# Optimization experiments

Hardware: AMD Instinct MI355X
Metric: run time of the kernel (lower is better)

Reference implementation:

```python
import jax, jax.numpy as jnp
import numpy as np

HS = WS = 1024      # downsampled mask dims (8192 / scale_factor 8)
K = 24              # kernel_num
KD = 35             # kernel_dim1 == kernel_dim2
OFF = HS // 2 - KD // 2  # offset_s = 495
MASK_STEEP = 4.0
MASK_SHIFT = 0.5
RESIST_STEEP = 50.0
RESIST_TH = 0.225
MAX_DOSE = 1.02
MIN_DOSE = 0.98
POOL = 3            # avepool_kernel


def setup_inputs() -> dict:
    key = jax.random.key(0)
    ks = jax.random.split(key, 7)
    return {
        "mask_s": jax.random.uniform(ks[0], (1, 1, HS, WS), dtype=jnp.float32),
        "kf_re": jax.random.normal(ks[1], (K, KD, KD), dtype=jnp.float32),
        "kf_im": jax.random.normal(ks[2], (K, KD, KD), dtype=jnp.float32),
        "kd_re": jax.random.normal(ks[3], (K, KD, KD), dtype=jnp.float32),
        "kd_im": jax.random.normal(ks[4], (K, KD, KD), dtype=jnp.float32),
        "kf_scale": jax.random.uniform(ks[5], (K, 1, 1), dtype=jnp.float32),
        "kd_scale": jax.random.uniform(ks[6], (K, 1, 1), dtype=jnp.float32),
    }


def _avgpool3(x):
    # AvgPool2d(kernel=3, stride=1, pad=1), count_include_pad=True -> always /9
    s = jax.lax.reduce_window(x, 0.0, jax.lax.add, (1, 1, POOL, POOL),
                              (1, 1, 1, 1),
                              [(0, 0), (0, 0), (POOL // 2, POOL // 2), (POOL // 2, POOL // 2)])
    return s / float(POOL * POOL)


def _dose_branch(crop, kernel, scale, dose):
    # crop: [1,1,KD,KD] complex ; kernel: [K,KD,KD] complex ; scale: [K,1,1]
    buf = jnp.zeros((1, K, HS, WS), dtype=jnp.complex64)
    buf = buf.at[:, :, OFF:OFF + KD, OFF:OFF + KD].set(crop * dose * kernel)
    img = jnp.fft.ifft2(buf)                      # [1,K,HS,WS] complex
    inten = (img.real * img.real + img.imag * img.imag) * scale
    inten = jnp.sum(inten, axis=1, keepdims=True)  # [1,1,HS,WS]
    return jax.nn.sigmoid(RESIST_STEEP * (inten - RESIST_TH))


def reference(mask_s, kf_re, kf_im, kd_re, kd_im, kf_scale, kd_scale):
    kf = jax.lax.complex(kf_re, kf_im)
    kd = jax.lax.complex(kd_re, kd_im)
    mask = jax.nn.sigmoid(MASK_STEEP * (_avgpool3(mask_s) - MASK_SHIFT))
    mf = jnp.fft.fftshift(jnp.fft.fft2(mask), axes=(-2, -1))  # [1,1,HS,WS]
    crop = mf[:, :, OFF:OFF + KD, OFF:OFF + KD]               # [1,1,KD,KD]
    x_nom = _dose_branch(crop, kf, kf_scale, 1.0)
    x_max = _dose_branch(crop, kf, kf_scale, MAX_DOSE)
    x_min = _dose_branch(crop, kd, kd_scale, MIN_DOSE)
    return x_nom, x_max, x_min
```

## Files before the change

kernel.cpp:

```cpp
#include <hip/hip_runtime.h>
#include <math.h>

#define HS 1024
#define WS 1024
#define KK 24
#define KD 35
#define NF 35
#define NDP 69
#define NGRP 16
#define CROW 42
#define NCHUNK 38
#define PRS 10

#define G_OFF    0u
#define CROP_OFF 286720u
#define D_OFF    296520u
#define ZERO_QWORDS 6055

__global__ __launch_bounds__(256) void k_maskG(const float* __restrict__ ms,
                                               float2* __restrict__ G,
                                               unsigned long long* __restrict__ zq) {
    __shared__ float cs[WS + 8];
    __shared__ float m[WS];
    __shared__ float2 part[252];
    const int x = blockIdx.x;
    const int t = threadIdx.x;

    if (x < 24) {
        int i = x * 256 + t;
        if (i < ZERO_QWORDS) zq[i] = 0ull;
    }
    {
        const int j = 4 * t;
        float4 b = *(const float4*)&ms[x * WS + j];
        float4 a = make_float4(0.f, 0.f, 0.f, 0.f);
        float4 d = make_float4(0.f, 0.f, 0.f, 0.f);
        if (x > 0)      a = *(const float4*)&ms[(x - 1) * WS + j];
        if (x < HS - 1) d = *(const float4*)&ms[(x + 1) * WS + j];
        float4 s;
        s.x = a.x + b.x + d.x;
        s.y = a.y + b.y + d.y;
        s.z = a.z + b.z + d.z;
        s.w = a.w + b.w + d.w;
        *(float4*)&cs[4 + j] = s;
        if (t == 0) { cs[3] = 0.0f; cs[4 + WS] = 0.0f; }
    }
    __syncthreads();
    {
        const int j = 4 * t;
        float4 c = *(const float4*)&cs[4 + j];
        float l = cs[3 + j];
        float r = cs[8 + j];
        float p0 = (l   + c.x + c.y) * (1.0f / 9.0f);
        float p1 = (c.x + c.y + c.z) * (1.0f / 9.0f);
        float p2 = (c.y + c.z + c.w) * (1.0f / 9.0f);
        float p3 = (c.z + c.w + r  ) * (1.0f / 9.0f);
        float4 mv;
        mv.x = 1.0f / (1.0f + expf(-4.0f * (p0 - 0.5f)));
        mv.y = 1.0f / (1.0f + expf(-4.0f * (p1 - 0.5f)));
        mv.z = 1.0f / (1.0f + expf(-4.0f * (p2 - 0.5f)));
        mv.w = 1.0f / (1.0f + expf(-4.0f * (p3 - 0.5f)));
        *(float4*)&m[j] = mv;
    }
    __syncthreads();
    if (t < 252) {
        const int qi = t / 14, seg = t % 14;
        float si, ci, ss, cc;
        sincospif(-(float)(qi * seg) * (1.0f / 512.0f), &si, &ci);
        sincospif(-(float)(qi * 14)  * (1.0f / 512.0f), &ss, &cc);
        const float s2 = (qi & 1) ? -1.0f : 1.0f;
        const int qm = qi & 3;
        const float er = (qm == 0) ? 1.0f : (qm == 2) ? -1.0f : 0.0f;
        const float ei = (qm == 1) ? -1.0f : (qm == 3) ? 1.0f : 0.0f;
        float wr = ci, wi = si;
        float re = 0.0f, im = 0.0f;
        for (int y = seg; y < 256; y += 14) {
            float m0 = m[y], m1 = m[y + 256], m2 = m[y + 512], m3 = m[y + 768];
            float A  = fmaf(s2, m2, m0);
            float Bv = fmaf(s2, m3, m1);
            float tre = fmaf(er, Bv, A);
            float tim = ei * Bv;
            re += tre * wr - tim * wi;
            im += tre * wi + tim * wr;
            float nr = wr * cc - wi * ss;
            wi = wr * ss + wi * cc;
            wr = nr;
        }
        part[t] = make_float2(re, im);
    }
    __syncthreads();
    if (t < 18) {
        float re = 0.0f, im = 0.0f;
        for (int s = 0; s < 14; ++s) { float2 p = part[t * 14 + s]; re += p.x; im += p.y; }
        G[(17 + t) * HS + x] = make_float2(re, im);
        if (t > 0) G[(17 - t) * HS + x] = make_float2(re, -im);
    }
}

__global__ __launch_bounds__(256) void k_crop(const float2* __restrict__ G,
                                              float2* __restrict__ crop) {
    __shared__ float2 g2[64];
    __shared__ float2 part[245];
    const int q  = blockIdx.x >> 4;
    const int xs = (blockIdx.x & 15) * 64;
    const int t  = threadIdx.x;
    if (t < 64) g2[t] = G[q * HS + xs + t];
    __syncthreads();
    if (t < 245) {
        const int p = t / 7, seg = t % 7;
        const int v = p - 17;
        float si, ci, ss, cc;
        sincospif((float)(v * (xs + seg)) * (1.0f / 512.0f), &si, &ci);
        sincospif((float)(v * 7)          * (1.0f / 512.0f), &ss, &cc);
        float wr = ci, wi = si;
        float re = 0.0f, im = 0.0f;
        for (int r = seg; r < 64; r += 7) {
            float2 gv = g2[r];
            re += gv.x * wr + gv.y * wi;
            im += gv.y * wr - gv.x * wi;
            float nr = wr * cc - wi * ss;
            wi = wr * ss + wi * cc;
            wr = nr;
        }
        part[t] = make_float2(re, im);
    }
    __syncthreads();
    if (t < NF) {
        float re = 0.0f, im = 0.0f;
        for (int s = 0; s < 7; ++s) { float2 p2 = part[t * 7 + s]; re += p2.x; im += p2.y; }
        float* dst = (float*)&crop[t * NF + q];
        atomicAdd(dst,     re);
        atomicAdd(dst + 1, im);
    }
}

__global__ __launch_bounds__(256) void k_D(
    const float2* __restrict__ crop,
    const float* __restrict__ kre0, const float* __restrict__ kim0,
    const float* __restrict__ kre1, const float* __restrict__ kim1,
    const float* __restrict__ sc0,  const float* __restrict__ sc1,
    float2* __restrict__ D)
{
    __shared__ float2 C[KD * CROW];
    __shared__ float partRf[2][NCHUNK * 6 * PRS];
    const int tup = blockIdx.x;
    const int t   = threadIdx.x;

    const int b   = tup / (KK * NGRP);
    const int rem = tup % (KK * NGRP);
    const int k   = rem / NGRP;
    const int g   = rem % NGRP;
    const float* kre = b ? kre1 : kre0;
    const float* kim = b ? kim1 : kim0;
    const float dosefac = (b ? 0.98f : 1.0f) * (1.0f / 1048576.0f);
    const float sk2 = ((b ? sc1 : sc0)[k]) * dosefac * dosefac;

    if (t < 245) C[(t / 7) * CROW + 35 + (t % 7)] = make_float2(0.0f, 0.0f);
    #pragma unroll
    for (int j = 0; j < 5; ++j) {
        int i = t + j * 256;
        if (i < KD * KD) {
            float2 c = crop[i];
            int row = i / 35, col = i % 35;
            float kr = kre[k * KD * KD + i], ki = kim[k * KD * KD + i];
            C[row * CROW + col] = make_float2(c.x * kr - c.y * ki,
                                              c.x * ki + c.y * kr);
        }
    }
    __syncthreads();

    const int ch = t / 6;
    const int pg = t % 6;
    const bool act = (ch < NCHUNK);
    const int tau = (ch >= 7) + (ch >= 14) + (ch >= 20) + (ch >= 25)
                  + (ch >= 29) + (ch >= 32) + (ch >= 35) + (ch >= 37);
    const int cbt = (tau == 0) ? 0 : (tau == 1) ? 7 : (tau == 2) ? 14 : (tau == 3) ? 20
                  : (tau == 4) ? 25 : (tau == 5) ? 29 : (tau == 6) ? 32 : (tau == 7) ? 35 : 37;
    const int d0 = 4 * tau;
    const int u0 = 5 * (ch - cbt);

    const int tau2 = t >> 2;
    const int cb2 = (tau2 == 0) ? 0 : (tau2 == 1) ? 7 : (tau2 == 2) ? 14 : (tau2 == 3) ? 20
                  : (tau2 == 4) ? 25 : (tau2 == 5) ? 29 : (tau2 == 6) ? 32 : (tau2 == 7) ? 35 : 37;
    const int cn2 = (tau2 == 0) ? 7 : (tau2 == 1) ? 7 : (tau2 == 2) ? 6 : (tau2 == 3) ? 5
                  : (tau2 == 4) ? 4 : (tau2 == 5) ? 3 : (tau2 == 6) ? 3 : (tau2 == 7) ? 2 : 1;
    const int s0 = cb2 * 6, cnt = cn2 * 6, c2 = (t & 3) * 2;

    int pb = 0;
    for (int idp = g; idp < NDP; idp += NGRP) {
        const int dp = idp - 34;
        if (act) {
            const int plo = max(0, dp), phi = min(34, 34 + dp);
            float2 ac0 = {0,0}, ac1 = {0,0}, ac2 = {0,0}, ac3 = {0,0};
            for (int p = plo + pg; p <= phi; p += 6) {
                const float2* rowa = &C[p * CROW + d0 + u0];
                const float2* rowb = &C[(p - dp) * CROW + u0];
                float2 a0 = rowa[0], a1 = rowa[1], a2 = rowa[2];
                #pragma unroll
                for (int s = 0; s < 5; ++s) {
                    float2 a3 = rowa[s + 3];
                    float2 bb = rowb[s];
                    ac0.x += a0.x * bb.x + a0.y * bb.y;  ac0.y += a0.y * bb.x - a0.x * bb.y;
                    ac1.x += a1.x * bb.x + a1.y * bb.y;  ac1.y += a1.y * bb.x - a1.x * bb.y;
                    ac2.x += a2.x * bb.x + a2.y * bb.y;  ac2.y += a2.y * bb.x - a2.x * bb.y;
                    ac3.x += a3.x * bb.x + a3.y * bb.y;  ac3.y += a3.y * bb.x - a3.x * bb.y;
                    a0 = a1; a1 = a2; a2 = a3;
                }
            }
            float* pr = &partRf[pb][t * PRS];
            *(float2*)&pr[0] = ac0;
            *(float2*)&pr[2] = ac1;
            *(float2*)&pr[4] = ac2;
            *(float2*)&pr[6] = ac3;
        }
        __syncthreads();
        if (t < NF) {
            float re = 0.0f, im = 0.0f;
            for (int j = 0; j < cnt; ++j) {
                const float2 v = *(const float2*)&partRf[pb][(s0 + j) * PRS + c2];
                re += v.x; im += v.y;
            }
            float* dst = (float*)&D[(b * NDP + idp) * NF + t];
            atomicAdd(dst,     re * sk2);
            atomicAdd(dst + 1, im * sk2);
        }
        pb ^= 1;
    }
}

__global__ __launch_bounds__(256) void k_final(const float2* __restrict__ D,
                                               float* __restrict__ out) {
    __shared__ float2 partB[210];
    __shared__ float2 B[NF][2];
    const int x = blockIdx.x;
    const int t = threadIdx.x;
    if (t < 210) {
        const int s = t / 70, r = t % 70, b = r / 35, dq = r % 35;
        float si, ci, ss, cc;
        sincospif((float)((23 * s - 34) * x) * (1.0f / 512.0f), &si, &ci);
        sincospif((float)x                   * (1.0f / 512.0f), &ss, &cc);
        float wr = ci, wi = si;
        float re = 0.0f, im = 0.0f;
        const int i0 = 23 * s;
        for (int idp = i0; idp < i0 + 23; ++idp) {
            float2 d = D[(b * NDP + idp) * NF + dq];
            re += d.x * wr - d.y * wi;
            im += d.x * wi + d.y * wr;
            float nr = wr * cc - wi * ss;
            wi = wr * ss + wi * cc;
            wr = nr;
        }
        partB[t] = make_float2(re, im);
    }
    __syncthreads();
    if (t < 70) {
        float2 a = partB[t], b2 = partB[t + 70], c = partB[t + 140];
        B[t % 35][t / 35] = make_float2(a.x + b2.x + c.x, a.y + b2.y + c.y);
    }
    __syncthreads();
    const float bf0 = B[0][0].x;
    const float bd0 = B[0][1].x;
    float s1, c1;
    sincospif((float)t * (1.0f / 512.0f), &s1, &c1);
    float cx = c1, cy = s1;
    float2 Sf[4] = {{0,0},{0,0},{0,0},{0,0}};
    float2 Sd[4] = {{0,0},{0,0},{0,0},{0,0}};
    #pragma unroll
    for (int dq = 1; dq < NF; ++dq) {
        const float2 bf = B[dq][0];
        const float2 bd = B[dq][1];
        const int mm = dq & 3;
        Sf[mm].x += bf.x * cx - bf.y * cy;
        Sf[mm].y += bf.x * cy + bf.y * cx;
        Sd[mm].x += bd.x * cx - bd.y * cy;
        Sd[mm].y += bd.x * cy + bd.y * cx;
        const float nx = cx * c1 - cy * s1;
        cy = cx * s1 + cy * c1;
        cx = nx;
    }
    float sf[4], sd[4];
    sf[0] = Sf[0].x + Sf[1].x + Sf[2].x + Sf[3].x;
    sf[1] = Sf[0].x - Sf[1].y - Sf[2].x + Sf[3].y;
    sf[2] = Sf[0].x - Sf[1].x + Sf[2].x - Sf[3].x;
    sf[3] = Sf[0].x + Sf[1].y - Sf[2].x - Sf[3].y;
    sd[0] = Sd[0].x + Sd[1].x + Sd[2].x + Sd[3].x;
    sd[1] = Sd[0].x - Sd[1].y - Sd[2].x + Sd[3].y;
    sd[2] = Sd[0].x - Sd[1].x + Sd[2].x - Sd[3].x;
    sd[3] = Sd[0].x + Sd[1].y - Sd[2].x - Sd[3].y;
    #pragma unroll
    for (int j = 0; j < 4; ++j) {
        const float If = bf0 + 2.0f * sf[j];
        const float Id = bd0 + 2.0f * sd[j];
        const int o = x * WS + t + 256 * j;
        out[o]               = 1.0f / (1.0f + expf(-50.0f * (If - 0.225f)));
        out[o + HS * WS]     = 1.0f / (1.0f + expf(-50.0f * (1.0404f * If - 0.225f)));
        out[o + 2 * HS * WS] = 1.0f / (1.0f + expf(-50.0f * (Id - 0.225f)));
    }
}

extern "C" void kernel_launch(void* const* d_in, const int* in_sizes, int n_in,
                              void* d_out, int out_size, void* d_ws, size_t ws_size,
                              hipStream_t stream) {
    (void)in_sizes; (void)n_in; (void)out_size; (void)ws_size;
    const float* ms    = (const float*)d_in[0];
    const float* kf_re = (const float*)d_in[1];
    const float* kf_im = (const float*)d_in[2];
    const float* kd_re = (const float*)d_in[3];
    const float* kd_im = (const float*)d_in[4];
    const float* kf_sc = (const float*)d_in[5];
    const float* kd_sc = (const float*)d_in[6];

    char* ws = (char*)d_ws;
    float2* G      = (float2*)(ws + G_OFF);
    float2* crop   = (float2*)(ws + CROP_OFF);
    float2* D      = (float2*)(ws + D_OFF);
    unsigned long long* zq = (unsigned long long*)(ws + CROP_OFF);
    float* out     = (float*)d_out;

    k_maskG<<<HS, 256, 0, stream>>>(ms, G, zq);
    k_crop<<<NF * 16, 256, 0, stream>>>(G, crop);
    k_D<<<2 * KK * NGRP, 256, 0, stream>>>(crop, kf_re, kf_im, kd_re, kd_im, kf_sc, kd_sc, D);
    k_final<<<HS, 256, 0, stream>>>(D, out);
}
```

Baseline: 48.94 us.

## Use Chebyshev twiddle recurrence, split crop blocks finer, spread D reduction across waves

```diff
diff --git a/kernel.cpp b/kernel.cpp
--- a/kernel.cpp
+++ b/kernel.cpp
@@ -72,7 +72,10 @@
         const int qm = qi & 3;
         const float er = (qm == 0) ? 1.0f : (qm == 2) ? -1.0f : 0.0f;
         const float ei = (qm == 1) ? -1.0f : (qm == 3) ? 1.0f : 0.0f;
+        const float tc = 2.0f * cc;
         float wr = ci, wi = si;
+        float pr = ci * cc + si * ss;
+        float pi = si * cc - ci * ss;
         float re = 0.0f, im = 0.0f;
         for (int y = seg; y < 256; y += 14) {
             float m0 = m[y], m1 = m[y + 256], m2 = m[y + 512], m3 = m[y + 768];
@@ -82,9 +85,9 @@
             float tim = ei * Bv;
             re += tre * wr - tim * wi;
             im += tre * wi + tim * wr;
-            float nr = wr * cc - wi * ss;
-            wi = wr * ss + wi * cc;
-            wr = nr;
+            float nr = tc * wr - pr;
+            float ni = tc * wi - pi;
+            pr = wr; pi = wi; wr = nr; wi = ni;
         }
         part[t] = make_float2(re, im);
     }
@@ -99,12 +102,12 @@
 
 __global__ __launch_bounds__(256) void k_crop(const float2* __restrict__ G,
                                               float2* __restrict__ crop) {
-    __shared__ float2 g2[64];
+    __shared__ float2 g2[32];
     __shared__ float2 part[245];
-    const int q  = blockIdx.x >> 4;
-    const int xs = (blockIdx.x & 15) * 64;
+    const int q  = blockIdx.x >> 5;
+    const int xs = (blockIdx.x & 31) * 32;
     const int t  = threadIdx.x;
-    if (t < 64) g2[t] = G[q * HS + xs + t];
+    if (t < 32) g2[t] = G[q * HS + xs + t];
     __syncthreads();
     if (t < 245) {
         const int p = t / 7, seg = t % 7;
@@ -112,15 +115,18 @@
         float si, ci, ss, cc;
         sincospif((float)(v * (xs + seg)) * (1.0f / 512.0f), &si, &ci);
         sincospif((float)(v * 7)          * (1.0f / 512.0f), &ss, &cc);
+        const float tc = 2.0f * cc;
         float wr = ci, wi = si;
-        float re = 0.0f, im = 0.0f;
-        for (int r = seg; r < 64; r += 7) {
+        float pr = ci * cc + si * ss;
+        float pi = si * cc - ci * ss;
+        float re = 0.0f, im = 0.0f;
+        for (int r = seg; r < 32; r += 7) {
             float2 gv = g2[r];
             re += gv.x * wr + gv.y * wi;
             im += gv.y * wr - gv.x * wi;
-            float nr = wr * cc - wi * ss;
-            wi = wr * ss + wi * cc;
-            wr = nr;
+            float nr = tc * wr - pr;
+            float ni = tc * wi - pi;
+            pr = wr; pi = wi; wr = nr; wi = ni;
         }
         part[t] = make_float2(re, im);
     }
@@ -179,12 +185,15 @@
     const int d0 = 4 * tau;
     const int u0 = 5 * (ch - cbt);
 
-    const int tau2 = t >> 2;
-    const int cb2 = (tau2 == 0) ? 0 : (tau2 == 1) ? 7 : (tau2 == 2) ? 14 : (tau2 == 3) ? 20
-                  : (tau2 == 4) ? 25 : (tau2 == 5) ? 29 : (tau2 == 6) ? 32 : (tau2 == 7) ? 35 : 37;
-    const int cn2 = (tau2 == 0) ? 7 : (tau2 == 1) ? 7 : (tau2 == 2) ? 6 : (tau2 == 3) ? 5
-                  : (tau2 == 4) ? 4 : (tau2 == 5) ? 3 : (tau2 == 6) ? 3 : (tau2 == 7) ? 2 : 1;
-    const int s0 = cb2 * 6, cnt = cn2 * 6, c2 = (t & 3) * 2;
+    const int w4 = t >> 6;
+    const int ix = t & 63;
+    const int dqr = 4 * ix + w4;
+    const bool ract = (ix < 9) && (dqr < NF);
+    const int cb2 = (ix == 0) ? 0 : (ix == 1) ? 7 : (ix == 2) ? 14 : (ix == 3) ? 20
+                  : (ix == 4) ? 25 : (ix == 5) ? 29 : (ix == 6) ? 32 : (ix == 7) ? 35 : 37;
+    const int cn2 = (ix == 0) ? 7 : (ix == 1) ? 7 : (ix == 2) ? 6 : (ix == 3) ? 5
+                  : (ix == 4) ? 4 : (ix == 5) ? 3 : (ix == 6) ? 3 : (ix == 7) ? 2 : 1;
+    const int s0 = cb2 * 6, cnt = cn2 * 6, c2 = w4 * 2;
 
     int pb = 0;
     for (int idp = g; idp < NDP; idp += NGRP) {
@@ -214,13 +223,13 @@
             *(float2*)&pr[6] = ac3;
         }
         __syncthreads();
-        if (t < NF) {
+        if (ract) {
             float re = 0.0f, im = 0.0f;
             for (int j = 0; j < cnt; ++j) {
                 const float2 v = *(const float2*)&partRf[pb][(s0 + j) * PRS + c2];
                 re += v.x; im += v.y;
             }
-            float* dst = (float*)&D[(b * NDP + idp) * NF + t];
+            float* dst = (float*)&D[(b * NDP + idp) * NF + dqr];
             atomicAdd(dst,     re * sk2);
             atomicAdd(dst + 1, im * sk2);
         }
@@ -239,16 +248,19 @@
         float si, ci, ss, cc;
         sincospif((float)((23 * s - 34) * x) * (1.0f / 512.0f), &si, &ci);
         sincospif((float)x                   * (1.0f / 512.0f), &ss, &cc);
+        const float tc = 2.0f * cc;
         float wr = ci, wi = si;
+        float pr = ci * cc + si * ss;
+        float pi = si * cc - ci * ss;
         float re = 0.0f, im = 0.0f;
         const int i0 = 23 * s;
         for (int idp = i0; idp < i0 + 23; ++idp) {
             float2 d = D[(b * NDP + idp) * NF + dq];
             re += d.x * wr - d.y * wi;
             im += d.x * wi + d.y * wr;
-            float nr = wr * cc - wi * ss;
-            wi = wr * ss + wi * cc;
-            wr = nr;
+            float nr = tc * wr - pr;
+            float ni = tc * wi - pi;
+            pr = wr; pi = wi; wr = nr; wi = ni;
         }
         partB[t] = make_float2(re, im);
     }
@@ -262,7 +274,9 @@
     const float bd0 = B[0][1].x;
     float s1, c1;
     sincospif((float)t * (1.0f / 512.0f), &s1, &c1);
+    const float tc = 2.0f * c1;
     float cx = c1, cy = s1;
+    float px = 1.0f, py = 0.0f;
     float2 Sf[4] = {{0,0},{0,0},{0,0},{0,0}};
     float2 Sd[4] = {{0,0},{0,0},{0,0},{0,0}};
     #pragma unroll
@@ -274,9 +288,9 @@
         Sf[mm].y += bf.x * cy + bf.y * cx;
         Sd[mm].x += bd.x * cx - bd.y * cy;
         Sd[mm].y += bd.x * cy + bd.y * cx;
-        const float nx = cx * c1 - cy * s1;
-        cy = cx * s1 + cy * c1;
-        cx = nx;
+        const float nx = tc * cx - px;
+        const float ny = tc * cy - py;
+        px = cx; py = cy; cx = nx; cy = ny;
     }
     float sf[4], sd[4];
     sf[0] = Sf[0].x + Sf[1].x + Sf[2].x + Sf[3].x;
@@ -318,7 +332,7 @@
     float* out     = (float*)d_out;
 
     k_maskG<<<HS, 256, 0, stream>>>(ms, G, zq);
-    k_crop<<<NF * 16, 256, 0, stream>>>(G, crop);
+    k_crop<<<NF * 32, 256, 0, stream>>>(G, crop);
     k_D<<<2 * KK * NGRP, 256, 0, stream>>>(crop, kf_re, kf_im, kd_re, kd_im, kf_sc, kd_sc, D);
     k_final<<<HS, 256, 0, stream>>>(D, out);
 }
```

Measured after the change: 63.29 us. 1.29x slower.
